# Kernel tuning notes

Hardware: AMD Instinct MI355X
Metric: run time of the kernel (lower is better)

The kernel has to match this reference:

```python
import jax, jax.numpy as jnp
import numpy as np

B, T, D_IN = 4, 512, 4096
H, G, HD = 32, 8, 128            # num_heads, num_kv_groups, head_dim
GS = H // G                      # group_size
CACHE = 3584                     # prev cache length (uniform across batch)
S = CACHE + T                    # total kv length
ROPE_BASE = 10000.0


def _rope_tables(max_pos, head_dim):
    inv_freq = 1.0 / (ROPE_BASE ** (jnp.arange(0, head_dim, 2, dtype=jnp.float32) / head_dim))
    angles = jnp.arange(max_pos, dtype=jnp.float32)[:, None] * inv_freq[None, :]  # [S, hd/2]
    angles = jnp.concatenate([angles, angles], axis=-1)                            # [S, hd]
    return jnp.cos(angles), jnp.sin(angles)


def apply_rope(x, cos, sin, start_positions):
    # x: [B, nH, T, hd]; cos/sin: [S, hd]; start_positions: [B] int
    t = x.shape[2]
    pos = start_positions[:, None] + jnp.arange(t)       # [B, T]
    c = cos[pos][:, None, :, :]                          # [B, 1, T, hd]
    s = sin[pos][:, None, :, :]
    x1, x2 = jnp.split(x, 2, axis=-1)
    rotated = jnp.concatenate([-x2, x1], axis=-1)
    return x * c + rotated * s


def setup_inputs() -> dict:
    key = jax.random.key(0)
    ks = jax.random.split(key, 8)
    x = jax.random.normal(ks[0], (B, T, D_IN), dtype=jnp.float32)
    cos, sin = _rope_tables(S, HD)
    start_positions = jnp.full((B,), CACHE, dtype=jnp.int32)
    # causal mask over absolute positions: query i sits at CACHE+i; True = masked
    kv_pos = jnp.arange(S)[None, None, None, :]
    q_pos = (CACHE + jnp.arange(T))[None, None, :, None]
    mask = jnp.broadcast_to(kv_pos > q_pos, (B, 1, T, S))
    prev_k = jax.random.normal(ks[1], (B, G, CACHE, HD), dtype=jnp.float32)
    prev_v = jax.random.normal(ks[2], (B, G, CACHE, HD), dtype=jnp.float32)
    sc = 0.02
    q_w = jax.random.normal(ks[3], (D_IN, H * HD), dtype=jnp.float32) * sc
    k_w = jax.random.normal(ks[4], (D_IN, G * HD), dtype=jnp.float32) * sc
    v_w = jax.random.normal(ks[5], (D_IN, G * HD), dtype=jnp.float32) * sc
    o_w = jax.random.normal(ks[6], (H * HD, H * HD), dtype=jnp.float32) * sc
    return {"x": x, "mask": mask, "cos": cos, "sin": sin,
            "start_positions": start_positions, "prev_k": prev_k, "prev_v": prev_v,
            "q_w": q_w, "k_w": k_w, "v_w": v_w, "o_w": o_w}


def reference(x, mask, cos, sin, start_positions, prev_k, prev_v, q_w, k_w, v_w, o_w):
    b, t, _ = x.shape
    q = (x @ q_w).reshape(b, t, H, HD).transpose(0, 2, 1, 3)   # [B,H,T,hd]
    k = (x @ k_w).reshape(b, t, G, HD).transpose(0, 2, 1, 3)   # [B,G,T,hd]
    v = (x @ v_w).reshape(b, t, G, HD).transpose(0, 2, 1, 3)   # [B,G,T,hd]
    q = apply_rope(q, cos, sin, start_positions)
    k = apply_rope(k, cos, sin, start_positions)
    # cache concat (uniform lengths -> padded batch concat)
    k_all = jnp.concatenate([prev_k, k], axis=2)               # [B,G,S,hd]
    v_all = jnp.concatenate([prev_v, v], axis=2)
    # GQA expansion: repeat each kv group for its group of query heads
    k_rep = jnp.repeat(k_all, GS, axis=1)                      # [B,H,S,hd]
    v_rep = jnp.repeat(v_all, GS, axis=1)
    scores = jnp.einsum('bhtd,bhsd->bhts', q, k_rep)
    scores = jnp.where(mask, -jnp.inf, scores)
    attn = jax.nn.softmax(scores / jnp.sqrt(jnp.asarray(HD, x.dtype)), axis=-1)
    ctx = jnp.einsum('bhts,bhsd->bthd', attn, v_rep).reshape(b, t, H * HD)
    out = ctx @ o_w
    return out, k_all, v_all
```

## Files before the change

kernel.cpp:

```cpp
#include <hip/hip_runtime.h>

#define B_     4
#define T_     512
#define DIN    4096
#define H_     32
#define G_     8
#define HD_    128
#define S_     4096
#define CACHE_ 3584
#define M_     2048
#define NQKV   6144
#define SCALE  0.08838834764831843f
#define LOG2E  1.4426950408889634f
#define QSC    (SCALE * LOG2E)

typedef __attribute__((ext_vector_type(4)))  float  f32x4;
typedef __attribute__((ext_vector_type(16))) float  f32x16;
typedef __attribute__((ext_vector_type(8)))  short  s16x8;
typedef __attribute__((ext_vector_type(4)))  unsigned short u16x4;
typedef __attribute__((ext_vector_type(8)))  unsigned short u16x8;
typedef __attribute__((ext_vector_type(4)))  unsigned int   u32x4;
typedef unsigned short u16;
typedef unsigned int   u32;

__device__ __forceinline__ u16 f2bf(float f) {
  u32 u = __builtin_bit_cast(u32, f);
  return (u16)((u + 0x7fffu + ((u >> 16) & 1u)) >> 16);
}
__device__ __forceinline__ float bf2f(u16 h) {
  return __builtin_bit_cast(float, (u32)h << 16);
}
__device__ __forceinline__ f32x4 mfma16(s16x8 a, s16x8 b, f32x4 c) {
  return __builtin_amdgcn_mfma_f32_16x16x32_bf16(a, b, c, 0, 0, 0);
}
__device__ __forceinline__ u32 pkbf(float a, float b) {
  u32 r; asm("v_cvt_pk_bf16_f32 %0, %1, %2" : "=v"(r) : "v"(a), "v"(b)); return r;
}
__device__ __forceinline__ void gload_lds16(const void* g, void* l) {
  __builtin_amdgcn_global_load_lds((__attribute__((address_space(1))) void*)g,
                                   (__attribute__((address_space(3))) void*)l, 16, 0, 0);
}

__global__ __launch_bounds__(256) void k_cvt_x(const float* __restrict__ x, u16* __restrict__ xb) {
  size_t i = ((size_t)blockIdx.x * 256 + threadIdx.x) * 4;
  f32x4 v = *(const f32x4*)(x + i);
  u16x4 o = { f2bf(v[0]), f2bf(v[1]), f2bf(v[2]), f2bf(v[3]) };
  *(u16x4*)(xb + i) = o;
}

__global__ __launch_bounds__(256) void k_twt(const float* __restrict__ src, int ldn,
                                             u16* __restrict__ dst) {
  __shared__ float tile[64][68];
  int k0 = blockIdx.x * 64, n0 = blockIdx.y * 64;
  int t = threadIdx.x;
  int rr = t >> 4, cc = (t & 15) * 4;
#pragma unroll
  for (int p = 0; p < 4; ++p) {
    int r = p * 16 + rr;
    f32x4 v = *(const f32x4*)(src + (size_t)(k0 + r) * ldn + n0 + cc);
    tile[r][cc] = v[0]; tile[r][cc + 1] = v[1]; tile[r][cc + 2] = v[2]; tile[r][cc + 3] = v[3];
  }
  __syncthreads();
#pragma unroll
  for (int p = 0; p < 4; ++p) {
    int n = p * 16 + rr;
    u16x4 o = { f2bf(tile[cc][n]), f2bf(tile[cc + 1][n]), f2bf(tile[cc + 2][n]), f2bf(tile[cc + 3][n]) };
    *(u16x4*)(dst + (size_t)(n0 + n) * 4096 + k0 + cc) = o;
  }
}

__global__ __launch_bounds__(256) void k_prep_k(const float* __restrict__ pk,
                                                float* __restrict__ k_all, u16* __restrict__ kb) {
  int bg = blockIdx.y;
  size_t si = ((size_t)blockIdx.x * 256 + threadIdx.x) * 4;
  f32x4 v = *(const f32x4*)(pk + (size_t)bg * CACHE_ * HD_ + si);
  size_t dof = (size_t)bg * S_ * HD_ + si;
  *(f32x4*)(k_all + dof) = v;
  u16x4 o = { f2bf(v[0]), f2bf(v[1]), f2bf(v[2]), f2bf(v[3]) };
  *(u16x4*)(kb + dof) = o;
}

__global__ __launch_bounds__(256) void k_prep_v(const float* __restrict__ pv,
                                                float* __restrict__ v_all, u16* __restrict__ vt) {
  __shared__ float tile[64][132];
  int bg = blockIdx.y, s0 = blockIdx.x * 64;
  int t = threadIdx.x;
  const float* src = pv + ((size_t)bg * CACHE_ + s0) * HD_;
  float* dc = v_all + ((size_t)bg * S_ + s0) * HD_;
  int r8 = t >> 5, c4 = (t & 31) * 4;
#pragma unroll
  for (int p = 0; p < 8; ++p) {
    int r = p * 8 + r8;
    f32x4 v = *(const f32x4*)(src + (size_t)r * HD_ + c4);
    *(f32x4*)(dc + (size_t)r * HD_ + c4) = v;
    tile[r][c4] = v[0]; tile[r][c4 + 1] = v[1]; tile[r][c4 + 2] = v[2]; tile[r][c4 + 3] = v[3];
  }
  __syncthreads();
  int hr = t >> 4, s4 = (t & 15) * 4;
#pragma unroll
  for (int p = 0; p < 8; ++p) {
    int hd = p * 16 + hr;
    u16x4 o = { f2bf(tile[s4][hd]), f2bf(tile[s4 + 1][hd]), f2bf(tile[s4 + 2][hd]), f2bf(tile[s4 + 3][hd]) };
    *(u16x4*)(vt + ((size_t)bg * HD_ + hd) * S_ + s0 + s4) = o;
  }
}

template<int BM, bool OUT_F32>
__global__ __launch_bounds__(512, 1) void k_gemm2(const u16* __restrict__ A, const u16* __restrict__ Bt,
                                                  void* __restrict__ Cp, int M, int N, int K) {
  constexpr int MI = BM / 32;
  constexpr int LA = BM / 64;
  __shared__ u16 As[2 * BM * 64];
  __shared__ u16 Bs[2 * 256 * 64];
  const int tid = threadIdx.x, w = tid >> 6, lane = tid & 63;
  const int wr = w >> 2, wc = w & 3;
  const int cl = lane & 15, khi = lane >> 4;
  const int Mt = M / BM;
  const int nwg = gridDim.x;
  const int q = nwg >> 3, r8 = nwg & 7;
  const int xcd = blockIdx.x & 7, pos = blockIdx.x >> 3;
  const int wgid = (xcd < r8 ? xcd * (q + 1) : r8 * (q + 1) + (xcd - r8) * q) + pos;
  const int m0 = (wgid % Mt) * BM, n0 = (wgid / Mt) * 256;
  const int rb = tid >> 3;
  const int csw = ((tid & 7) ^ (rb & 7)) * 8;
  const u16* aS = A  + (size_t)(m0 + rb) * K + csw;
  const u16* bS = Bt + (size_t)(n0 + rb) * K + csw;
  u16* aD = As + w * 512;
  u16* bD = Bs + w * 512;
  const int ck0 = ((0 + khi) ^ (cl & 7)) * 8;
  const int ck1 = ((4 + khi) ^ (cl & 7)) * 8;
  const int NT = K >> 6;
  f32x4 acc[MI][4] = {};

#define STAGE_(buf, tt)                                                                   \
  do {                                                                                    \
    _Pragma("unroll")                                                                     \
    for (int i = 0; i < LA; ++i)                                                          \
      gload_lds16(aS + (size_t)(i * 64) * K + (size_t)(tt) * 64, aD + (buf) * (BM * 64) + i * 4096); \
    _Pragma("unroll")                                                                     \
    for (int i = 0; i < 4; ++i)                                                           \
      gload_lds16(bS + (size_t)(i * 64) * K + (size_t)(tt) * 64, bD + (buf) * (256 * 64) + i * 4096); \
  } while (0)
#define VMCNT_L_()                                                                        \
  do {                                                                                    \
    if constexpr (BM == 256) asm volatile("s_waitcnt vmcnt(8)" ::: "memory");             \
    else                     asm volatile("s_waitcnt vmcnt(6)" ::: "memory");             \
  } while (0)

  STAGE_(0, 0);
  STAGE_(1, 1);
  VMCNT_L_();
  __builtin_amdgcn_sched_barrier(0);
  __builtin_amdgcn_s_barrier();
  __builtin_amdgcn_sched_barrier(0);

  for (int t = 0; t < NT; ++t) {
    const int buf = t & 1;
    const int ab = buf * (BM * 64) + (wr * (BM / 2) + cl) * 64;
    const int bb = buf * (256 * 64) + (wc * 64 + cl) * 64;
#pragma unroll
    for (int kk = 0; kk < 2; ++kk) {
      const int ck = kk ? ck1 : ck0;
      s16x8 bf4[4], af[MI];
#pragma unroll
      for (int ni = 0; ni < 4; ++ni) bf4[ni] = *(const s16x8*)(Bs + bb + ni * 16 * 64 + ck);
#pragma unroll
      for (int mi = 0; mi < MI; ++mi) af[mi] = *(const s16x8*)(As + ab + mi * 16 * 64 + ck);
      __builtin_amdgcn_s_setprio(1);
#pragma unroll
      for (int mi = 0; mi < MI; ++mi)
#pragma unroll
        for (int ni = 0; ni < 4; ++ni)
          acc[mi][ni] = mfma16(af[mi], bf4[ni], acc[mi][ni]);
      __builtin_amdgcn_s_setprio(0);
    }
    __builtin_amdgcn_sched_barrier(0);
    __builtin_amdgcn_s_barrier();
    __builtin_amdgcn_sched_barrier(0);
    if (t + 2 < NT) STAGE_(buf, t + 2);
    VMCNT_L_();
    __builtin_amdgcn_sched_barrier(0);
    __builtin_amdgcn_s_barrier();
    __builtin_amdgcn_sched_barrier(0);
  }
#undef STAGE_
#undef VMCNT_L_
  const int rl = khi * 4;
#pragma unroll
  for (int mi = 0; mi < MI; ++mi)
#pragma unroll
    for (int ni = 0; ni < 4; ++ni) {
      int col = n0 + wc * 64 + ni * 16 + cl;
#pragma unroll
      for (int r = 0; r < 4; ++r) {
        int rw = m0 + wr * (BM / 2) + mi * 16 + rl + r;
        if (OUT_F32) ((float*)Cp)[(size_t)rw * N + col] = acc[mi][ni][r];
        else         ((u16*)Cp)[(size_t)rw * N + col]   = f2bf(acc[mi][ni][r]);
      }
    }
}

__global__ __launch_bounds__(256) void k_rope(const u16* __restrict__ qkv, const float* __restrict__ cosT,
                                              const float* __restrict__ sinT, const int* __restrict__ sp,
                                              u16* __restrict__ qr, u16* __restrict__ kb,
                                              float* __restrict__ k_all, float* __restrict__ v_all) {
  int bt = blockIdx.x;
  int b = bt >> 9, t = bt & 511;
  int pos = sp[b] + t;
  const u16* row = qkv + (size_t)bt * NQKV;
  for (int idx = threadIdx.x; idx < 2560; idx += 256) {
    int head = idx >> 6, d = idx & 63;
    float c = cosT[pos * HD_ + d], s = sinT[pos * HD_ + d];
    float x1 = bf2f(row[head * HD_ + d]);
    float x2 = bf2f(row[head * HD_ + d + 64]);
    float y1 = x1 * c - x2 * s;
    float y2 = x2 * c + x1 * s;
    if (head < 32) {
      size_t o = (((size_t)b * H_ + head) * T_ + t) * HD_ + d;
      qr[o] = f2bf(y1 * QSC); qr[o + 64] = f2bf(y2 * QSC);
    } else {
      int g = head - 32;
      size_t o = (((size_t)b * G_ + g) * S_ + CACHE_ + t) * HD_ + d;
      kb[o] = f2bf(y1); kb[o + 64] = f2bf(y2);
      k_all[o] = y1; k_all[o + 64] = y2;
    }
  }
  for (int idx = threadIdx.x; idx < 1024; idx += 256) {
    int g = idx >> 7;
    float v = bf2f(row[5120 + idx]);
    size_t o = (((size_t)b * G_ + g) * S_ + CACHE_ + t) * HD_ + (idx & 127);
    v_all[o] = v;
  }
}

__global__ __launch_bounds__(256) void k_tv_new(const u16* __restrict__ qkv, u16* __restrict__ vt) {
  __shared__ u16 tile[64][72];
  int bg = blockIdx.y;
  int b = bg >> 3, g = bg & 7;
  int tt = blockIdx.x >> 1, ht = blockIdx.x & 1;
  int t0 = tt * 64, hd0 = ht * 64;
  int t = threadIdx.x;
  int rr = t >> 3, c8 = (t & 7) * 8;
#pragma unroll
  for (int p = 0; p < 2; ++p) {
    int r = p * 32 + rr;
    *(u16x8*)(&tile[r][c8]) =
      *(const u16x8*)(qkv + (size_t)(b * T_ + t0 + r) * NQKV + 5120 + g * HD_ + hd0 + c8);
  }
  __syncthreads();
  int hr = t >> 4, s4 = (t & 15) * 4;
#pragma unroll
  for (int p = 0; p < 4; ++p) {
    int hd = p * 16 + hr;
    u16x4 o = { tile[s4][hd], tile[s4 + 1][hd], tile[s4 + 2][hd], tile[s4 + 3][hd] };
    *(u16x4*)(vt + ((size_t)bg * HD_ + hd0 + hd) * S_ + CACHE_ + t0 + s4) = o;
  }
}

__global__ __launch_bounds__(512, 2) void k_attn(const u16* __restrict__ Q, const u16* __restrict__ Kc,
                                                 const u16* __restrict__ Vt, const int* __restrict__ sp,
                                                 u16* __restrict__ ctx) {
  __shared__ u16 Ks[64 * 128];
  __shared__ u16 Vs[128 * 64];
  const int qh = blockIdx.x, h = blockIdx.y, b = blockIdx.z;
  const int g = h >> 2;
  const int tid = threadIdx.x, w = tid >> 6, lane = tid & 63;
  const int l31 = lane & 31, hh = lane >> 5;
  const int cache = sp[b];
  const int qbase = qh * 256;
  const int qtok = qbase + w * 32 + l31;
  const size_t kvoff = (size_t)(b * G_ + g) * S_ * HD_;
  const u16* kp = Kc + kvoff;
  const u16* vp = Vt + kvoff;
  s16x8 qreg[8];
  {
    const u16* qb = Q + ((size_t)(b * H_ + h) * T_ + qtok) * HD_;
#pragma unroll
    for (int s = 0; s < 8; ++s) qreg[s] = *(const s16x8*)(qb + s * 16 + hh * 8);
  }
  f32x16 acc[4] = {};
  float mr = -1e30f, ls = 0.f;
  const int krow = w * 8 + (lane >> 3), kch = lane & 7;
  const int vrow = w * 16 + (lane >> 2), vch = lane & 3;
  const int kswz = (krow & 15) << 3;
  const int vswz = (vrow & 7) << 3;
  const int rdswzK = (l31 & 15) << 3;
  const int rdswzV = (l31 & 7) << 3;
  const int jm = (cache + qbase + w * 32) >> 6;
  const int jlastB = (cache + qbase + 255) >> 6;
  const int kvlim = cache + qtok;
  u16x8 rk0 = *(const u16x8*)(kp + (size_t)krow * HD_ + kch * 8);
  u16x8 rk1 = *(const u16x8*)(kp + (size_t)krow * HD_ + (kch + 8) * 8);
  u16x8 rv0 = *(const u16x8*)(vp + (size_t)vrow * S_ + vch * 8);
  u16x8 rv1 = *(const u16x8*)(vp + (size_t)vrow * S_ + (vch + 4) * 8);
  for (int j = 0; j <= jlastB; ++j) {
    __syncthreads();
    *(u16x8*)(Ks + krow * 128 + ((kch * 8) ^ kswz))        = rk0;
    *(u16x8*)(Ks + krow * 128 + (((kch + 8) * 8) ^ kswz))  = rk1;
    *(u16x8*)(Vs + vrow * 64 + ((vch * 8) ^ vswz))         = rv0;
    *(u16x8*)(Vs + vrow * 64 + (((vch + 4) * 8) ^ vswz))   = rv1;
    __syncthreads();
    if (j < jlastB) {
      rk0 = *(const u16x8*)(kp + (size_t)((j + 1) * 64 + krow) * HD_ + kch * 8);
      rk1 = *(const u16x8*)(kp + (size_t)((j + 1) * 64 + krow) * HD_ + (kch + 8) * 8);
      rv0 = *(const u16x8*)(vp + (size_t)vrow * S_ + (j + 1) * 64 + vch * 8);
      rv1 = *(const u16x8*)(vp + (size_t)vrow * S_ + (j + 1) * 64 + vch * 8 + 32);
    }
    f32x16 sa[2] = {};
#pragma unroll
    for (int s = 0; s < 8; ++s) {
      s16x8 ka = *(const s16x8*)(Ks + l31 * 128 + ((s * 16 + hh * 8) ^ rdswzK));
      sa[0] = __builtin_amdgcn_mfma_f32_32x32x16_bf16(ka, qreg[s], sa[0], 0, 0, 0);
    }
#pragma unroll
    for (int s = 0; s < 8; ++s) {
      s16x8 ka = *(const s16x8*)(Ks + (32 + l31) * 128 + ((s * 16 + hh * 8) ^ rdswzK));
      sa[1] = __builtin_amdgcn_mfma_f32_32x32x16_bf16(ka, qreg[s], sa[1], 0, 0, 0);
    }
    if (j >= jm) {
#pragma unroll
      for (int r = 0; r < 16; ++r) {
        int kv = j * 64 + (r & 3) + 8 * (r >> 2) + 4 * hh;
        if (kv > kvlim)      sa[0][r] = -1e30f;
        if (kv + 32 > kvlim) sa[1][r] = -1e30f;
      }
    }
    float mx = sa[0][0];
#pragma unroll
    for (int r = 1; r < 16; ++r) mx = fmaxf(mx, sa[0][r]);
#pragma unroll
    for (int r = 0; r < 16; ++r) mx = fmaxf(mx, sa[1][r]);
    mx = fmaxf(mx, __shfl_xor(mx, 32));
    if (__any(mx > mr + 8.f)) {
      float nm = fmaxf(mr, mx);
      float al = __builtin_amdgcn_exp2f(mr - nm);
      mr = nm; ls *= al;
#pragma unroll
      for (int r = 0; r < 16; ++r) {
        float ar = __shfl(al, (r & 3) + 8 * (r >> 2) + 4 * hh, 64);
        acc[0][r] *= ar; acc[1][r] *= ar; acc[2][r] *= ar; acc[3][r] *= ar;
      }
    }
    float rs = 0.f;
#pragma unroll
    for (int r = 0; r < 16; ++r) { sa[0][r] = __builtin_amdgcn_exp2f(sa[0][r] - mr); rs += sa[0][r]; }
#pragma unroll
    for (int r = 0; r < 16; ++r) { sa[1][r] = __builtin_amdgcn_exp2f(sa[1][r] - mr); rs += sa[1][r]; }
    rs += __shfl_xor(rs, 32);
    ls += rs;
    s16x8 pf[4];
#pragma unroll
    for (int sb = 0; sb < 2; ++sb) {
      u32 a0 = pkbf(sa[sb][0],  sa[sb][1]),  a1 = pkbf(sa[sb][2],  sa[sb][3]);
      u32 b0 = pkbf(sa[sb][4],  sa[sb][5]),  b1 = pkbf(sa[sb][6],  sa[sb][7]);
      u32 c0 = pkbf(sa[sb][8],  sa[sb][9]),  c1 = pkbf(sa[sb][10], sa[sb][11]);
      u32 d0 = pkbf(sa[sb][12], sa[sb][13]), d1 = pkbf(sa[sb][14], sa[sb][15]);
      u32 xa0 = __shfl_xor(a0, 32), xa1 = __shfl_xor(a1, 32);
      u32 xb0 = __shfl_xor(b0, 32), xb1 = __shfl_xor(b1, 32);
      u32 xc0 = __shfl_xor(c0, 32), xc1 = __shfl_xor(c1, 32);
      u32 xd0 = __shfl_xor(d0, 32), xd1 = __shfl_xor(d1, 32);
      u32x4 f0 = { hh ? xb0 : a0, hh ? xb1 : a1, hh ? b0 : xa0, hh ? b1 : xa1 };
      u32x4 f1 = { hh ? xd0 : c0, hh ? xd1 : c1, hh ? d0 : xc0, hh ? d1 : xc1 };
      pf[sb * 2]     = __builtin_bit_cast(s16x8, f0);
      pf[sb * 2 + 1] = __builtin_bit_cast(s16x8, f1);
    }
#pragma unroll
    for (int hb = 0; hb < 4; ++hb) {
      const int vro = hb * 32 + l31;
#pragma unroll
      for (int kb = 0; kb < 4; ++kb) {
        s16x8 vb = *(const s16x8*)(Vs + vro * 64 + ((kb * 16 + hh * 8) ^ rdswzV));
        acc[hb] = __builtin_amdgcn_mfma_f32_32x32x16_bf16(pf[kb], vb, acc[hb], 0, 0, 0);
      }
    }
  }
  float inv = 1.0f / ls;
#pragma unroll
  for (int r = 0; r < 16; ++r) {
    int ql = (r & 3) + 8 * (r >> 2) + 4 * hh;
    float ivr = __shfl(inv, ql, 64);
    u16* cb = ctx + ((size_t)(b * T_ + qbase + w * 32 + ql)) * 4096 + h * HD_ + l31;
    cb[0]  = f2bf(acc[0][r] * ivr);
    cb[32] = f2bf(acc[1][r] * ivr);
    cb[64] = f2bf(acc[2][r] * ivr);
    cb[96] = f2bf(acc[3][r] * ivr);
  }
}

extern "C" void kernel_launch(void* const* d_in, const int* in_sizes, int n_in,
                              void* d_out, int out_size, void* d_ws, size_t ws_size,
                              hipStream_t stream) {
  const float* x      = (const float*)d_in[0];
  const float* cosT   = (const float*)d_in[2];
  const float* sinT   = (const float*)d_in[3];
  const int*   sp     = (const int*)d_in[4];
  const float* prev_k = (const float*)d_in[5];
  const float* prev_v = (const float*)d_in[6];
  const float* q_w    = (const float*)d_in[7];
  const float* k_w    = (const float*)d_in[8];
  const float* v_w    = (const float*)d_in[9];
  const float* o_w    = (const float*)d_in[10];

  float* out   = (float*)d_out;
  float* k_all = out + (size_t)B_ * T_ * H_ * HD_;
  float* v_all = k_all + (size_t)B_ * G_ * S_ * HD_;

  char* w = (char*)d_ws;
  u16* wt_qkv = (u16*)(w);
  u16* wt_o   = (u16*)(w + 50331648);
  u16* x_bf   = (u16*)(w + 83886080);
  u16* qkv_bf = (u16*)(w + 100663296);
  u16* q_rope = (u16*)(w + 125829120);
  u16* k_bf   = (u16*)(w + 142606336);
  u16* v_t    = (u16*)(w + 176160768);
  u16* ctx    = (u16*)(w + 209715200);
  if (ws_size < 226492416ull) return;

  k_cvt_x<<<8192, 256, 0, stream>>>(x, x_bf);
  k_twt<<<dim3(64, 64), 256, 0, stream>>>(q_w, 4096, wt_qkv);
  k_twt<<<dim3(64, 16), 256, 0, stream>>>(k_w, 1024, wt_qkv + (size_t)4096 * 4096);
  k_twt<<<dim3(64, 16), 256, 0, stream>>>(v_w, 1024, wt_qkv + (size_t)5120 * 4096);
  k_twt<<<dim3(64, 64), 256, 0, stream>>>(o_w, 4096, wt_o);
  k_prep_k<<<dim3(448, 32), 256, 0, stream>>>(prev_k, k_all, k_bf);
  k_prep_v<<<dim3(56, 32), 256, 0, stream>>>(prev_v, v_all, v_t);
  k_gemm2<256, false><<<192, 512, 0, stream>>>(x_bf, wt_qkv, qkv_bf, M_, NQKV, 4096);
  k_rope<<<2048, 256, 0, stream>>>(qkv_bf, cosT, sinT, sp, q_rope, k_bf, k_all, v_all);
  k_tv_new<<<dim3(16, 32), 256, 0, stream>>>(qkv_bf, v_t);
  k_attn<<<dim3(2, 32, 4), 512, 0, stream>>>(q_rope, k_bf, v_t, sp, ctx);
  k_gemm2<128, true><<<256, 512, 0, stream>>>(ctx, wt_o, out, M_, 4096, 4096);
}
```

Measured before the change: 541.3 us.

## Double-buffer attention K/V via direct global-to-LDS loads with XCD-aware block mapping

The attention kernel now uses 256-thread blocks covering 128 queries each, giving 512 blocks instead of 256. A 1D grid is remapped so that blocks sharing a KV group land on the same XCD for L2 reuse. K/V tiles are staged with async global-to-LDS loads into two buffers, prefetching two tiles ahead. This replaces the register round trip and double syncthreads. MFMA sections get raised wave priority, and the smaller per-block query count means each block rereads the K/V stream, roughly doubling K/V traffic through L2.

After: 690.0 us. +27.5%, slower.

```diff
diff --git a/kernel.cpp b/kernel.cpp
--- a/kernel.cpp
+++ b/kernel.cpp
@@ -257,19 +257,21 @@
   }
 }
 
-__global__ __launch_bounds__(512, 2) void k_attn(const u16* __restrict__ Q, const u16* __restrict__ Kc,
-                                                 const u16* __restrict__ Vt, const int* __restrict__ sp,
-                                                 u16* __restrict__ ctx) {
-  __shared__ u16 Ks[64 * 128];
-  __shared__ u16 Vs[128 * 64];
-  const int qh = blockIdx.x, h = blockIdx.y, b = blockIdx.z;
-  const int g = h >> 2;
+__global__ __launch_bounds__(256) void k_attn(const u16* __restrict__ Q, const u16* __restrict__ Kc,
+                                              const u16* __restrict__ Vt, const int* __restrict__ sp,
+                                              u16* __restrict__ ctx) {
+  __shared__ u16 Ks[2][64 * 128];
+  __shared__ u16 Vs[2][128 * 64];
+  const int xcd = blockIdx.x & 7, pos = blockIdx.x >> 3;
+  const int wgid = xcd * 64 + pos;
+  const int qh = wgid & 3, hq = (wgid >> 2) & 3, bg = wgid >> 4;
+  const int b = bg >> 3, g = bg & 7, h = g * 4 + hq;
   const int tid = threadIdx.x, w = tid >> 6, lane = tid & 63;
   const int l31 = lane & 31, hh = lane >> 5;
   const int cache = sp[b];
-  const int qbase = qh * 256;
+  const int qbase = qh * 128;
   const int qtok = qbase + w * 32 + l31;
-  const size_t kvoff = (size_t)(b * G_ + g) * S_ * HD_;
+  const size_t kvoff = (size_t)bg * S_ * HD_;
   const u16* kp = Kc + kvoff;
   const u16* vp = Vt + kvoff;
   s16x8 qreg[8];
@@ -280,43 +282,51 @@
   }
   f32x16 acc[4] = {};
   float mr = -1e30f, ls = 0.f;
-  const int krow = w * 8 + (lane >> 3), kch = lane & 7;
-  const int vrow = w * 16 + (lane >> 2), vch = lane & 3;
-  const int kswz = (krow & 15) << 3;
-  const int vswz = (vrow & 7) << 3;
+  const int tr   = tid >> 4;
+  const int kcol = ((tid & 15) ^ tr) * 8;
+  const int vrw  = tid >> 3;
+  const int vcol = ((tid & 7) ^ (vrw & 7)) * 8;
+  const int dB   = w * 512;
   const int rdswzK = (l31 & 15) << 3;
   const int rdswzV = (l31 & 7) << 3;
   const int jm = (cache + qbase + w * 32) >> 6;
-  const int jlastB = (cache + qbase + 255) >> 6;
+  const int jlastB = (cache + qbase + 127) >> 6;
   const int kvlim = cache + qtok;
-  u16x8 rk0 = *(const u16x8*)(kp + (size_t)krow * HD_ + kch * 8);
-  u16x8 rk1 = *(const u16x8*)(kp + (size_t)krow * HD_ + (kch + 8) * 8);
-  u16x8 rv0 = *(const u16x8*)(vp + (size_t)vrow * S_ + vch * 8);
-  u16x8 rv1 = *(const u16x8*)(vp + (size_t)vrow * S_ + (vch + 4) * 8);
+
+#define ASTAGE_(bufi, jj)                                                                  \
+  do {                                                                                     \
+    _Pragma("unroll")                                                                      \
+    for (int i = 0; i < 4; ++i)                                                            \
+      gload_lds16(kp + (size_t)((jj) * 64 + i * 16 + tr) * HD_ + kcol, &Ks[bufi][i * 2048 + dB]); \
+    _Pragma("unroll")                                                                      \
+    for (int i = 0; i < 4; ++i)                                                            \
+      gload_lds16(vp + (size_t)(i * 32 + vrw) * S_ + (jj) * 64 + vcol, &Vs[bufi][i * 2048 + dB]); \
+  } while (0)
+
+  ASTAGE_(0, 0);
+  ASTAGE_(1, 1);
+  asm volatile("s_waitcnt vmcnt(8)" ::: "memory");
+  __builtin_amdgcn_sched_barrier(0);
+  __builtin_amdgcn_s_barrier();
+  __builtin_amdgcn_sched_barrier(0);
+
   for (int j = 0; j <= jlastB; ++j) {
-    __syncthreads();
-    *(u16x8*)(Ks + krow * 128 + ((kch * 8) ^ kswz))        = rk0;
-    *(u16x8*)(Ks + krow * 128 + (((kch + 8) * 8) ^ kswz))  = rk1;
-    *(u16x8*)(Vs + vrow * 64 + ((vch * 8) ^ vswz))         = rv0;
-    *(u16x8*)(Vs + vrow * 64 + (((vch + 4) * 8) ^ vswz))   = rv1;
-    __syncthreads();
-    if (j < jlastB) {
-      rk0 = *(const u16x8*)(kp + (size_t)((j + 1) * 64 + krow) * HD_ + kch * 8);
-      rk1 = *(const u16x8*)(kp + (size_t)((j + 1) * 64 + krow) * HD_ + (kch + 8) * 8);
-      rv0 = *(const u16x8*)(vp + (size_t)vrow * S_ + (j + 1) * 64 + vch * 8);
-      rv1 = *(const u16x8*)(vp + (size_t)vrow * S_ + (j + 1) * 64 + vch * 8 + 32);
-    }
+    const int buf = j & 1;
+    const u16* KsB = Ks[buf];
+    const u16* VsB = Vs[buf];
     f32x16 sa[2] = {};
+    __builtin_amdgcn_s_setprio(1);
 #pragma unroll
     for (int s = 0; s < 8; ++s) {
-      s16x8 ka = *(const s16x8*)(Ks + l31 * 128 + ((s * 16 + hh * 8) ^ rdswzK));
+      s16x8 ka = *(const s16x8*)(KsB + l31 * 128 + ((s * 16 + hh * 8) ^ rdswzK));
       sa[0] = __builtin_amdgcn_mfma_f32_32x32x16_bf16(ka, qreg[s], sa[0], 0, 0, 0);
     }
 #pragma unroll
     for (int s = 0; s < 8; ++s) {
-      s16x8 ka = *(const s16x8*)(Ks + (32 + l31) * 128 + ((s * 16 + hh * 8) ^ rdswzK));
+      s16x8 ka = *(const s16x8*)(KsB + (32 + l31) * 128 + ((s * 16 + hh * 8) ^ rdswzK));
       sa[1] = __builtin_amdgcn_mfma_f32_32x32x16_bf16(ka, qreg[s], sa[1], 0, 0, 0);
     }
+    __builtin_amdgcn_s_setprio(0);
     if (j >= jm) {
 #pragma unroll
       for (int r = 0; r < 16; ++r) {
@@ -364,16 +374,27 @@
       pf[sb * 2]     = __builtin_bit_cast(s16x8, f0);
       pf[sb * 2 + 1] = __builtin_bit_cast(s16x8, f1);
     }
+    __builtin_amdgcn_s_setprio(1);
 #pragma unroll
     for (int hb = 0; hb < 4; ++hb) {
       const int vro = hb * 32 + l31;
 #pragma unroll
       for (int kb = 0; kb < 4; ++kb) {
-        s16x8 vb = *(const s16x8*)(Vs + vro * 64 + ((kb * 16 + hh * 8) ^ rdswzV));
+        s16x8 vb = *(const s16x8*)(VsB + vro * 64 + ((kb * 16 + hh * 8) ^ rdswzV));
         acc[hb] = __builtin_amdgcn_mfma_f32_32x32x16_bf16(pf[kb], vb, acc[hb], 0, 0, 0);
       }
     }
-  }
+    __builtin_amdgcn_s_setprio(0);
+    __builtin_amdgcn_sched_barrier(0);
+    __builtin_amdgcn_s_barrier();
+    __builtin_amdgcn_sched_barrier(0);
+    ASTAGE_(buf, (j + 2 <= jlastB) ? (j + 2) : jlastB);
+    asm volatile("s_waitcnt vmcnt(8)" ::: "memory");
+    __builtin_amdgcn_sched_barrier(0);
+    __builtin_amdgcn_s_barrier();
+    __builtin_amdgcn_sched_barrier(0);
+  }
+#undef ASTAGE_
   float inv = 1.0f / ls;
 #pragma unroll
   for (int r = 0; r < 16; ++r) {
@@ -426,6 +447,6 @@
   k_gemm2<256, false><<<192, 512, 0, stream>>>(x_bf, wt_qkv, qkv_bf, M_, NQKV, 4096);
   k_rope<<<2048, 256, 0, stream>>>(qkv_bf, cosT, sinT, sp, q_rope, k_bf, k_all, v_all);
   k_tv_new<<<dim3(16, 32), 256, 0, stream>>>(qkv_bf, v_t);
-  k_attn<<<dim3(2, 32, 4), 512, 0, stream>>>(q_rope, k_bf, v_t, sp, ctx);
+  k_attn<<<512, 256, 0, stream>>>(q_rope, k_bf, v_t, sp, ctx);
   k_gemm2<128, true><<<256, 512, 0, stream>>>(ctx, wt_o, out, M_, 4096, 4096);
 }
```

## Split attention into 128-query blocks with XCD-aware GQA mapping and MFMA priority

Applied to the files above, without the earlier changes.

The attention kernel now launches 512 blocks of 256 threads, each covering 128 queries, instead of 256 blocks of 512 threads covering 256 queries. A flat block index is remapped so that the blocks sharing one KV group land on the same XCD, which should let them reuse K/V in that XCD's L2. Thread-to-tile load mappings are changed so each thread stages four 16-byte chunks, and s_setprio raises wave priority around the MFMA sections. Smaller query tiles improve load balance and occupancy, but each KV tile is fetched by more blocks overall.

Measured after the change: 632.0 us. 1.17x slower.

```diff
diff --git a/kernel.cpp b/kernel.cpp
--- a/kernel.cpp
+++ b/kernel.cpp
@@ -257,19 +257,21 @@
   }
 }
 
-__global__ __launch_bounds__(512, 2) void k_attn(const u16* __restrict__ Q, const u16* __restrict__ Kc,
-                                                 const u16* __restrict__ Vt, const int* __restrict__ sp,
-                                                 u16* __restrict__ ctx) {
+__global__ __launch_bounds__(256) void k_attn(const u16* __restrict__ Q, const u16* __restrict__ Kc,
+                                              const u16* __restrict__ Vt, const int* __restrict__ sp,
+                                              u16* __restrict__ ctx) {
   __shared__ u16 Ks[64 * 128];
   __shared__ u16 Vs[128 * 64];
-  const int qh = blockIdx.x, h = blockIdx.y, b = blockIdx.z;
-  const int g = h >> 2;
+  const int xcd = blockIdx.x & 7, pos = blockIdx.x >> 3;
+  const int wgid = xcd * 64 + pos;
+  const int qh = wgid & 3, hq = (wgid >> 2) & 3, bg = wgid >> 4;
+  const int b = bg >> 3, g = bg & 7, h = g * 4 + hq;
   const int tid = threadIdx.x, w = tid >> 6, lane = tid & 63;
   const int l31 = lane & 31, hh = lane >> 5;
   const int cache = sp[b];
-  const int qbase = qh * 256;
+  const int qbase = qh * 128;
   const int qtok = qbase + w * 32 + l31;
-  const size_t kvoff = (size_t)(b * G_ + g) * S_ * HD_;
+  const size_t kvoff = (size_t)bg * S_ * HD_;
   const u16* kp = Kc + kvoff;
   const u16* vp = Vt + kvoff;
   s16x8 qreg[8];
@@ -280,33 +282,36 @@
   }
   f32x16 acc[4] = {};
   float mr = -1e30f, ls = 0.f;
-  const int krow = w * 8 + (lane >> 3), kch = lane & 7;
-  const int vrow = w * 16 + (lane >> 2), vch = lane & 3;
-  const int kswz = (krow & 15) << 3;
-  const int vswz = (vrow & 7) << 3;
+  const int kr = tid >> 2, kc = (tid & 3) * 4, kswz = kr & 15;
+  const int vr = tid >> 1, vc = (tid & 1) * 4, vswz = vr & 7;
   const int rdswzK = (l31 & 15) << 3;
   const int rdswzV = (l31 & 7) << 3;
   const int jm = (cache + qbase + w * 32) >> 6;
-  const int jlastB = (cache + qbase + 255) >> 6;
+  const int jlastB = (cache + qbase + 127) >> 6;
   const int kvlim = cache + qtok;
-  u16x8 rk0 = *(const u16x8*)(kp + (size_t)krow * HD_ + kch * 8);
-  u16x8 rk1 = *(const u16x8*)(kp + (size_t)krow * HD_ + (kch + 8) * 8);
-  u16x8 rv0 = *(const u16x8*)(vp + (size_t)vrow * S_ + vch * 8);
-  u16x8 rv1 = *(const u16x8*)(vp + (size_t)vrow * S_ + (vch + 4) * 8);
+  u16x8 rk[4], rv[4];
+#pragma unroll
+  for (int i = 0; i < 4; ++i) {
+    rk[i] = *(const u16x8*)(kp + (size_t)kr * HD_ + (kc + i) * 8);
+    rv[i] = *(const u16x8*)(vp + (size_t)vr * S_ + (vc + i) * 8);
+  }
   for (int j = 0; j <= jlastB; ++j) {
     __syncthreads();
-    *(u16x8*)(Ks + krow * 128 + ((kch * 8) ^ kswz))        = rk0;
-    *(u16x8*)(Ks + krow * 128 + (((kch + 8) * 8) ^ kswz))  = rk1;
-    *(u16x8*)(Vs + vrow * 64 + ((vch * 8) ^ vswz))         = rv0;
-    *(u16x8*)(Vs + vrow * 64 + (((vch + 4) * 8) ^ vswz))   = rv1;
+#pragma unroll
+    for (int i = 0; i < 4; ++i) {
+      *(u16x8*)(Ks + kr * 128 + ((kc + i) ^ kswz) * 8) = rk[i];
+      *(u16x8*)(Vs + vr * 64 + ((vc + i) ^ vswz) * 8)  = rv[i];
+    }
     __syncthreads();
     if (j < jlastB) {
-      rk0 = *(const u16x8*)(kp + (size_t)((j + 1) * 64 + krow) * HD_ + kch * 8);
-      rk1 = *(const u16x8*)(kp + (size_t)((j + 1) * 64 + krow) * HD_ + (kch + 8) * 8);
-      rv0 = *(const u16x8*)(vp + (size_t)vrow * S_ + (j + 1) * 64 + vch * 8);
-      rv1 = *(const u16x8*)(vp + (size_t)vrow * S_ + (j + 1) * 64 + vch * 8 + 32);
+#pragma unroll
+      for (int i = 0; i < 4; ++i) {
+        rk[i] = *(const u16x8*)(kp + (size_t)((j + 1) * 64 + kr) * HD_ + (kc + i) * 8);
+        rv[i] = *(const u16x8*)(vp + (size_t)vr * S_ + (j + 1) * 64 + (vc + i) * 8);
+      }
     }
     f32x16 sa[2] = {};
+    __builtin_amdgcn_s_setprio(1);
 #pragma unroll
     for (int s = 0; s < 8; ++s) {
       s16x8 ka = *(const s16x8*)(Ks + l31 * 128 + ((s * 16 + hh * 8) ^ rdswzK));
@@ -317,6 +322,7 @@
       s16x8 ka = *(const s16x8*)(Ks + (32 + l31) * 128 + ((s * 16 + hh * 8) ^ rdswzK));
       sa[1] = __builtin_amdgcn_mfma_f32_32x32x16_bf16(ka, qreg[s], sa[1], 0, 0, 0);
     }
+    __builtin_amdgcn_s_setprio(0);
     if (j >= jm) {
 #pragma unroll
       for (int r = 0; r < 16; ++r) {
@@ -364,6 +370,7 @@
       pf[sb * 2]     = __builtin_bit_cast(s16x8, f0);
       pf[sb * 2 + 1] = __builtin_bit_cast(s16x8, f1);
     }
+    __builtin_amdgcn_s_setprio(1);
 #pragma unroll
     for (int hb = 0; hb < 4; ++hb) {
       const int vro = hb * 32 + l31;
@@ -373,6 +380,7 @@
         acc[hb] = __builtin_amdgcn_mfma_f32_32x32x16_bf16(pf[kb], vb, acc[hb], 0, 0, 0);
       }
     }
+    __builtin_amdgcn_s_setprio(0);
   }
   float inv = 1.0f / ls;
 #pragma unroll
@@ -426,6 +434,6 @@
   k_gemm2<256, false><<<192, 512, 0, stream>>>(x_bf, wt_qkv, qkv_bf, M_, NQKV, 4096);
   k_rope<<<2048, 256, 0, stream>>>(qkv_bf, cosT, sinT, sp, q_rope, k_bf, k_all, v_all);
   k_tv_new<<<dim3(16, 32), 256, 0, stream>>>(qkv_bf, v_t);
-  k_attn<<<dim3(2, 32, 4), 512, 0, stream>>>(q_rope, k_bf, v_t, sp, ctx);
+  k_attn<<<512, 256, 0, stream>>>(q_rope, k_bf, v_t, sp, ctx);
   k_gemm2<128, true><<<256, 512, 0, stream>>>(ctx, wt_o, out, M_, 4096, 4096);
 }
```

## Double-buffer attention K/V tiles, remap blocks for XCD-local KV reuse, add setprio

Applied to the files above, without the earlier changes.

The attention kernel now keeps two LDS buffers for K and V tiles. The next tile is written to the alternate buffer while the current one is consumed, which leaves one barrier per iteration, and global prefetch runs two tiles ahead. The grid is flattened to 1D and remapped so that all blocks sharing a KV group (both query halves and the four heads) land on the same XCD, improving L2 reuse. It also adds s_setprio around the MFMA sections and uses a tree-shaped max reduction. The cost is double the LDS footprint and a dropped min-blocks launch bound, which may lower occupancy.

Result: no change. 541.3 us (+0.0%).

```diff
diff --git a/kernel.cpp b/kernel.cpp
--- a/kernel.cpp
+++ b/kernel.cpp
@@ -257,19 +257,21 @@
   }
 }
 
-__global__ __launch_bounds__(512, 2) void k_attn(const u16* __restrict__ Q, const u16* __restrict__ Kc,
-                                                 const u16* __restrict__ Vt, const int* __restrict__ sp,
-                                                 u16* __restrict__ ctx) {
-  __shared__ u16 Ks[64 * 128];
-  __shared__ u16 Vs[128 * 64];
-  const int qh = blockIdx.x, h = blockIdx.y, b = blockIdx.z;
-  const int g = h >> 2;
+__global__ __launch_bounds__(512) void k_attn(const u16* __restrict__ Q, const u16* __restrict__ Kc,
+                                              const u16* __restrict__ Vt, const int* __restrict__ sp,
+                                              u16* __restrict__ ctx) {
+  __shared__ u16 Ks[2][64 * 128];
+  __shared__ u16 Vs[2][128 * 64];
+  const int xcd = blockIdx.x & 7, pos = blockIdx.x >> 3;
+  const int wgid = xcd * 32 + pos;
+  const int qh = wgid & 1, hq = (wgid >> 1) & 3, bg = wgid >> 3;
+  const int b = bg >> 3, g = bg & 7, h = g * 4 + hq;
   const int tid = threadIdx.x, w = tid >> 6, lane = tid & 63;
   const int l31 = lane & 31, hh = lane >> 5;
   const int cache = sp[b];
   const int qbase = qh * 256;
   const int qtok = qbase + w * 32 + l31;
-  const size_t kvoff = (size_t)(b * G_ + g) * S_ * HD_;
+  const size_t kvoff = (size_t)bg * S_ * HD_;
   const u16* kp = Kc + kvoff;
   const u16* vp = Vt + kvoff;
   s16x8 qreg[8];
@@ -289,33 +291,50 @@
   const int jm = (cache + qbase + w * 32) >> 6;
   const int jlastB = (cache + qbase + 255) >> 6;
   const int kvlim = cache + qtok;
-  u16x8 rk0 = *(const u16x8*)(kp + (size_t)krow * HD_ + kch * 8);
-  u16x8 rk1 = *(const u16x8*)(kp + (size_t)krow * HD_ + (kch + 8) * 8);
-  u16x8 rv0 = *(const u16x8*)(vp + (size_t)vrow * S_ + vch * 8);
-  u16x8 rv1 = *(const u16x8*)(vp + (size_t)vrow * S_ + (vch + 4) * 8);
+  u16x8 rk0, rk1, rv0, rv1;
+  rk0 = *(const u16x8*)(kp + (size_t)krow * HD_ + kch * 8);
+  rk1 = *(const u16x8*)(kp + (size_t)krow * HD_ + (kch + 8) * 8);
+  rv0 = *(const u16x8*)(vp + (size_t)vrow * S_ + vch * 8);
+  rv1 = *(const u16x8*)(vp + (size_t)vrow * S_ + (vch + 4) * 8);
+  *(u16x8*)(Ks[0] + krow * 128 + ((kch * 8) ^ kswz))       = rk0;
+  *(u16x8*)(Ks[0] + krow * 128 + (((kch + 8) * 8) ^ kswz)) = rk1;
+  *(u16x8*)(Vs[0] + vrow * 64 + ((vch * 8) ^ vswz))        = rv0;
+  *(u16x8*)(Vs[0] + vrow * 64 + (((vch + 4) * 8) ^ vswz))  = rv1;
+  rk0 = *(const u16x8*)(kp + (size_t)(64 + krow) * HD_ + kch * 8);
+  rk1 = *(const u16x8*)(kp + (size_t)(64 + krow) * HD_ + (kch + 8) * 8);
+  rv0 = *(const u16x8*)(vp + (size_t)vrow * S_ + 64 + vch * 8);
+  rv1 = *(const u16x8*)(vp + (size_t)vrow * S_ + 64 + (vch + 4) * 8);
+  __syncthreads();
   for (int j = 0; j <= jlastB; ++j) {
-    __syncthreads();
-    *(u16x8*)(Ks + krow * 128 + ((kch * 8) ^ kswz))        = rk0;
-    *(u16x8*)(Ks + krow * 128 + (((kch + 8) * 8) ^ kswz))  = rk1;
-    *(u16x8*)(Vs + vrow * 64 + ((vch * 8) ^ vswz))         = rv0;
-    *(u16x8*)(Vs + vrow * 64 + (((vch + 4) * 8) ^ vswz))   = rv1;
-    __syncthreads();
+    const int buf = j & 1;
+    const u16* KsB = Ks[buf];
+    const u16* VsB = Vs[buf];
+    u16* Ksn = Ks[buf ^ 1];
+    u16* Vsn = Vs[buf ^ 1];
+    f32x16 sa[2] = {};
+    __builtin_amdgcn_s_setprio(1);
+#pragma unroll
+    for (int s = 0; s < 8; ++s) {
+      s16x8 ka = *(const s16x8*)(KsB + l31 * 128 + ((s * 16 + hh * 8) ^ rdswzK));
+      sa[0] = __builtin_amdgcn_mfma_f32_32x32x16_bf16(ka, qreg[s], sa[0], 0, 0, 0);
+    }
+#pragma unroll
+    for (int s = 0; s < 8; ++s) {
+      s16x8 ka = *(const s16x8*)(KsB + (32 + l31) * 128 + ((s * 16 + hh * 8) ^ rdswzK));
+      sa[1] = __builtin_amdgcn_mfma_f32_32x32x16_bf16(ka, qreg[s], sa[1], 0, 0, 0);
+    }
+    __builtin_amdgcn_s_setprio(0);
     if (j < jlastB) {
-      rk0 = *(const u16x8*)(kp + (size_t)((j + 1) * 64 + krow) * HD_ + kch * 8);
-      rk1 = *(const u16x8*)(kp + (size_t)((j + 1) * 64 + krow) * HD_ + (kch + 8) * 8);
-      rv0 = *(const u16x8*)(vp + (size_t)vrow * S_ + (j + 1) * 64 + vch * 8);
-      rv1 = *(const u16x8*)(vp + (size_t)vrow * S_ + (j + 1) * 64 + vch * 8 + 32);
-    }
-    f32x16 sa[2] = {};
-#pragma unroll
-    for (int s = 0; s < 8; ++s) {
-      s16x8 ka = *(const s16x8*)(Ks + l31 * 128 + ((s * 16 + hh * 8) ^ rdswzK));
-      sa[0] = __builtin_amdgcn_mfma_f32_32x32x16_bf16(ka, qreg[s], sa[0], 0, 0, 0);
-    }
-#pragma unroll
-    for (int s = 0; s < 8; ++s) {
-      s16x8 ka = *(const s16x8*)(Ks + (32 + l31) * 128 + ((s * 16 + hh * 8) ^ rdswzK));
-      sa[1] = __builtin_amdgcn_mfma_f32_32x32x16_bf16(ka, qreg[s], sa[1], 0, 0, 0);
+      *(u16x8*)(Ksn + krow * 128 + ((kch * 8) ^ kswz))       = rk0;
+      *(u16x8*)(Ksn + krow * 128 + (((kch + 8) * 8) ^ kswz)) = rk1;
+      *(u16x8*)(Vsn + vrow * 64 + ((vch * 8) ^ vswz))        = rv0;
+      *(u16x8*)(Vsn + vrow * 64 + (((vch + 4) * 8) ^ vswz))  = rv1;
+    }
+    if (j + 2 <= jlastB) {
+      rk0 = *(const u16x8*)(kp + (size_t)((j + 2) * 64 + krow) * HD_ + kch * 8);
+      rk1 = *(const u16x8*)(kp + (size_t)((j + 2) * 64 + krow) * HD_ + (kch + 8) * 8);
+      rv0 = *(const u16x8*)(vp + (size_t)vrow * S_ + (j + 2) * 64 + vch * 8);
+      rv1 = *(const u16x8*)(vp + (size_t)vrow * S_ + (j + 2) * 64 + (vch + 4) * 8);
     }
     if (j >= jm) {
 #pragma unroll
@@ -325,12 +344,21 @@
         if (kv + 32 > kvlim) sa[1][r] = -1e30f;
       }
     }
-    float mx = sa[0][0];
-#pragma unroll
-    for (int r = 1; r < 16; ++r) mx = fmaxf(mx, sa[0][r]);
-#pragma unroll
-    for (int r = 0; r < 16; ++r) mx = fmaxf(mx, sa[1][r]);
-    mx = fmaxf(mx, __shfl_xor(mx, 32));
+    float mx;
+    {
+      float t[16];
+#pragma unroll
+      for (int r = 0; r < 16; ++r) t[r] = fmaxf(sa[0][r], sa[1][r]);
+#define F3_(a, b, c) fmaxf(fmaxf(a, b), c)
+      float u0 = F3_(t[0], t[1], t[2]);
+      float u1 = F3_(t[3], t[4], t[5]);
+      float u2 = F3_(t[6], t[7], t[8]);
+      float u3 = F3_(t[9], t[10], t[11]);
+      float u4 = F3_(t[12], t[13], t[14]);
+      float lm = fmaxf(F3_(u0, u1, u2), F3_(u3, u4, t[15]));
+#undef F3_
+      mx = fmaxf(lm, __shfl_xor(lm, 32));
+    }
     if (__any(mx > mr + 8.f)) {
       float nm = fmaxf(mr, mx);
       float al = __builtin_amdgcn_exp2f(mr - nm);
@@ -364,15 +392,18 @@
       pf[sb * 2]     = __builtin_bit_cast(s16x8, f0);
       pf[sb * 2 + 1] = __builtin_bit_cast(s16x8, f1);
     }
+    __builtin_amdgcn_s_setprio(1);
 #pragma unroll
     for (int hb = 0; hb < 4; ++hb) {
       const int vro = hb * 32 + l31;
 #pragma unroll
       for (int kb = 0; kb < 4; ++kb) {
-        s16x8 vb = *(const s16x8*)(Vs + vro * 64 + ((kb * 16 + hh * 8) ^ rdswzV));
+        s16x8 vb = *(const s16x8*)(VsB + vro * 64 + ((kb * 16 + hh * 8) ^ rdswzV));
         acc[hb] = __builtin_amdgcn_mfma_f32_32x32x16_bf16(pf[kb], vb, acc[hb], 0, 0, 0);
       }
     }
+    __builtin_amdgcn_s_setprio(0);
+    __syncthreads();
   }
   float inv = 1.0f / ls;
 #pragma unroll
@@ -426,6 +457,6 @@
   k_gemm2<256, false><<<192, 512, 0, stream>>>(x_bf, wt_qkv, qkv_bf, M_, NQKV, 4096);
   k_rope<<<2048, 256, 0, stream>>>(qkv_bf, cosT, sinT, sp, q_rope, k_bf, k_all, v_all);
   k_tv_new<<<dim3(16, 32), 256, 0, stream>>>(qkv_bf, v_t);
-  k_attn<<<dim3(2, 32, 4), 512, 0, stream>>>(q_rope, k_bf, v_t, sp, ctx);
+  k_attn<<<256, 512, 0, stream>>>(q_rope, k_bf, v_t, sp, ctx);
   k_gemm2<128, true><<<256, 512, 0, stream>>>(ctx, wt_o, out, M_, 4096, 4096);
 }
```
